# Kernel tuning notes

Hardware: AMD Instinct MI355X
Metric: run time of the kernel (lower is better)

The kernel has to match this reference:

```python
import jax, jax.numpy as jnp
import numpy as np

RADIUS = 0.1
MAX_GRID_DIM = 96
MAX_COLLISIONS = 128
INCLUDE_SELF = True


def setup_inputs() -> dict:
    key = jax.random.key(0)
    k1, k2, k3 = jax.random.split(key, 3)
    B, N, M, D, C = 2, 8192, 8192, 3, 64
    locs = jax.random.uniform(k1, (B, N, D), dtype=jnp.float32)
    data = jax.random.normal(k2, (B, N, C), dtype=jnp.float32)
    qlocs = jax.random.uniform(k3, (B, M, D), dtype=jnp.float32)
    return {"locs": locs, "data": data, "qlocs": qlocs}


def _hashgrid_order(locs):
    """Returns idxs [B,N] int32 sorting particles by flattened hash-grid cell id.
       idxs[b,i] = original index of the particle at new position i."""
    lower = jnp.min(locs, axis=1, keepdims=True)          # [B,1,D]
    upper = jnp.max(locs, axis=1, keepdims=True)          # [B,1,D]
    # grid dims per batch/dim, cell width = radius, capped at max_grid_dim
    gd = jnp.clip(jnp.floor((upper - lower) / RADIUS).astype(jnp.int32) + 1,
                  1, MAX_GRID_DIM)                        # [B,1,D]
    cell = jnp.floor((locs - lower) / RADIUS).astype(jnp.int32)
    cell = jnp.clip(cell, 0, gd - 1)                      # [B,N,D]
    # mixed-radix flatten: stride[d] = prod(gd[d+1:])
    strides = jnp.concatenate(
        [jnp.cumprod(gd[..., ::-1], axis=-1)[..., ::-1][..., 1:],
         jnp.ones_like(gd[..., :1])], axis=-1)            # [B,1,D]
    cid = jnp.sum(cell * strides, axis=-1)                # [B,N]
    return jnp.argsort(cid, axis=1, stable=True).astype(jnp.int32)


def _collisions(qlocs, nlocs):
    """For each query, indices into reordered locs within RADIUS, lowest-index
       first, padded with -1 up to MAX_COLLISIONS. Returns [B,M,K] int32."""
    B, N, _ = nlocs.shape
    d2 = jnp.sum((qlocs[:, :, None, :] - nlocs[:, None, :, :]) ** 2, axis=-1)  # [B,M,N]
    mask = d2 <= RADIUS * RADIUS
    if not INCLUDE_SELF:
        mask = mask & (d2 > 0)
    # key = particle index if neighbor else N (sentinel); first K after sort
    key = jnp.where(mask, jnp.arange(N, dtype=jnp.int32)[None, None, :], N)
    first_k = jnp.sort(key, axis=-1)[..., :MAX_COLLISIONS]                     # [B,M,K]
    return jnp.where(first_k < N, first_k, -1).astype(jnp.int32)


def reference(locs, data, qlocs):
    idxs = _hashgrid_order(locs)                              # [B,N]
    nlocs = jnp.take_along_axis(locs, idxs[..., None], axis=1)   # reordered locs
    ndata = jnp.take_along_axis(data, idxs[..., None], axis=1)   # reordered data
    neighbors = _collisions(qlocs, nlocs)                     # [B,M,K]
    return nlocs, ndata, idxs, neighbors
```

## Files before the change

kernel.cpp:

```cpp
#include <hip/hip_runtime.h>
#include <cfloat>
#include <math.h>

#define BB 2
#define NN 8192
#define MM 8192
#define CC 64
#define RAD 0.1f
#define R2 0.01f
#define MAXK 128
#define CELL_CAP 4096
#define CS_STRIDE 4100

#define WS_HDR 0
#define WS_SIDX 32
#define WS_CS (WS_SIDX + BB*NN)

#define NEIGH_BLOCKS ((BB*MM*16)/256)
#define DATA_BLOCKS ((BB*NN*16)/256)
#define NLOC_BLOCKS ((BB*NN)/256)

__device__ __forceinline__ int cell_of(float v, float lo, int g) {
    int c = (int)floorf(__fdiv_rn(v - lo, RAD));
    return min(max(c, 0), g - 1);
}

__global__ __launch_bounds__(1024) void build_kernel(const float* __restrict__ locs,
                                                     int* __restrict__ ws,
                                                     float* __restrict__ idxs_out) {
    const int b = blockIdx.x;
    const int t = threadIdx.x;
    const int lane = t & 63;
    const int wid = t >> 6;
    __shared__ int s_start[CELL_CAP + 1];
    __shared__ int s_aux[16];
    __shared__ int s_tmp[NN];
    __shared__ int s_cid[NN];
    __shared__ float s_red6[16 * 6];
    __shared__ float s_lo[3];
    __shared__ int   s_g[3];
    __shared__ int   s_str[2];

    const float* L = locs + (size_t)b * NN * 3;

    float mn0 = FLT_MAX, mn1 = FLT_MAX, mn2 = FLT_MAX;
    float mx0 = -FLT_MAX, mx1 = -FLT_MAX, mx2 = -FLT_MAX;
    for (int i = t; i < NN; i += 1024) {
        float x = L[i*3+0], y = L[i*3+1], z = L[i*3+2];
        mn0 = fminf(mn0, x); mx0 = fmaxf(mx0, x);
        mn1 = fminf(mn1, y); mx1 = fmaxf(mx1, y);
        mn2 = fminf(mn2, z); mx2 = fmaxf(mx2, z);
    }
    #pragma unroll
    for (int d = 1; d < 64; d <<= 1) {
        mn0 = fminf(mn0, __shfl_xor(mn0, d, 64));
        mn1 = fminf(mn1, __shfl_xor(mn1, d, 64));
        mn2 = fminf(mn2, __shfl_xor(mn2, d, 64));
        mx0 = fmaxf(mx0, __shfl_xor(mx0, d, 64));
        mx1 = fmaxf(mx1, __shfl_xor(mx1, d, 64));
        mx2 = fmaxf(mx2, __shfl_xor(mx2, d, 64));
    }
    if (lane == 0) {
        s_red6[wid*6+0] = mn0; s_red6[wid*6+1] = mn1; s_red6[wid*6+2] = mn2;
        s_red6[wid*6+3] = mx0; s_red6[wid*6+4] = mx1; s_red6[wid*6+5] = mx2;
    }
    for (int c = t; c < CELL_CAP + 1; c += 1024) s_start[c] = 0;
    __syncthreads();
    if (t == 0) {
        float lo0 = FLT_MAX, lo1 = FLT_MAX, lo2 = FLT_MAX;
        float up0 = -FLT_MAX, up1 = -FLT_MAX, up2 = -FLT_MAX;
        for (int w = 0; w < 16; ++w) {
            lo0 = fminf(lo0, s_red6[w*6+0]); lo1 = fminf(lo1, s_red6[w*6+1]);
            lo2 = fminf(lo2, s_red6[w*6+2]);
            up0 = fmaxf(up0, s_red6[w*6+3]); up1 = fmaxf(up1, s_red6[w*6+4]);
            up2 = fmaxf(up2, s_red6[w*6+5]);
        }
        int g0 = min(max((int)floorf(__fdiv_rn(up0 - lo0, RAD)) + 1, 1), 96);
        int g1 = min(max((int)floorf(__fdiv_rn(up1 - lo1, RAD)) + 1, 1), 96);
        int g2 = min(max((int)floorf(__fdiv_rn(up2 - lo2, RAD)) + 1, 1), 96);
        s_lo[0] = lo0; s_lo[1] = lo1; s_lo[2] = lo2;
        s_g[0] = g0; s_g[1] = g1; s_g[2] = g2;
        s_str[0] = g1 * g2; s_str[1] = g2;
        int* hdr = ws + WS_HDR + b * 16;
        hdr[0] = __float_as_int(lo0); hdr[1] = __float_as_int(lo1); hdr[2] = __float_as_int(lo2);
        hdr[3] = g0; hdr[4] = g1; hdr[5] = g2;
        hdr[6] = g1 * g2; hdr[7] = g2; hdr[8] = g0 * g1 * g2;
    }
    __syncthreads();
    const float lo0 = s_lo[0], lo1 = s_lo[1], lo2f = s_lo[2];
    const int g0 = s_g[0], g1 = s_g[1], g2 = s_g[2];
    const int st0 = s_str[0], st1 = s_str[1];
    const int ncells = g0 * g1 * g2;

    for (int i = t; i < NN; i += 1024) {
        int c0 = cell_of(L[i*3+0], lo0, g0);
        int c1 = cell_of(L[i*3+1], lo1, g1);
        int c2 = cell_of(L[i*3+2], lo2f, g2);
        int cid = c0*st0 + c1*st1 + c2;
        s_cid[i] = cid;
        atomicAdd(&s_start[cid], 1);
    }
    __syncthreads();

    int base4 = t * 4;
    int v0 = s_start[base4], v1 = s_start[base4+1], v2 = s_start[base4+2], v3 = s_start[base4+3];
    int sum = v0 + v1 + v2 + v3;
    int x = sum;
    #pragma unroll
    for (int d = 1; d < 64; d <<= 1) {
        int v = __shfl_up(x, d, 64);
        if (lane >= d) x += v;
    }
    if (lane == 63) s_aux[wid] = x;
    __syncthreads();
    if (wid == 0) {
        int w = (lane < 16) ? s_aux[lane] : 0;
        #pragma unroll
        for (int d = 1; d < 16; d <<= 1) {
            int v = __shfl_up(w, d, 64);
            if (lane >= d) w += v;
        }
        if (lane < 16) s_aux[lane] = w;
    }
    __syncthreads();
    int waveoff = (wid == 0) ? 0 : s_aux[wid - 1];
    int run = waveoff + x - sum;
    s_start[base4]   = run;
    s_start[base4+1] = run + v0;
    s_start[base4+2] = run + v0 + v1;
    s_start[base4+3] = run + v0 + v1 + v2;
    if (t == 1023) s_start[CELL_CAP] = run + sum;
    __syncthreads();

    for (int i = t; i < NN; i += 1024) {
        int pos = atomicAdd(&s_start[s_cid[i]], 1);
        s_tmp[pos] = i;
    }
    __syncthreads();

    int* cs = ws + WS_CS + b * CS_STRIDE;
    for (int c = t; c <= ncells; c += 1024) cs[c] = (c == 0) ? 0 : s_start[c - 1];

    int* sIdx = ws + WS_SIDX + b * NN;
    for (int p = t; p < NN; p += 1024) {
        int i = s_tmp[p];
        int cid = s_cid[i];
        int segs = (cid == 0) ? 0 : s_start[cid - 1];
        int sege = s_start[cid];
        int rank = 0;
        for (int q = segs; q < sege; ++q) rank += (s_tmp[q] < i) ? 1 : 0;
        int f = segs + rank;
        sIdx[f] = i;
        idxs_out[b * NN + f] = (float)i;
    }
}

__global__ __launch_bounds__(256) void fused_kernel(const float4* __restrict__ data4,
                                                    const float* __restrict__ locs,
                                                    const float* __restrict__ qlocs,
                                                    const int* __restrict__ ws,
                                                    float4* __restrict__ ndata4,
                                                    float* __restrict__ nlocs_out,
                                                    float* __restrict__ neigh_out) {
    int bid = blockIdx.x;
    if (bid >= NEIGH_BLOCKS) {
        int gb = bid - NEIGH_BLOCKS;
        if (gb < DATA_BLOCKS) {
            int tid = gb * 256 + threadIdx.x;
            int b = tid >> 17;
            int r = tid & ((NN * 16) - 1);
            int p = r >> 4;
            int c4 = r & 15;
            int idx = ws[WS_SIDX + b * NN + p];
            ndata4[tid] = data4[(((size_t)b * NN + idx) << 4) + c4];
        } else {
            int u = (gb - DATA_BLOCKS) * 256 + threadIdx.x;
            int b = u >> 13;
            int p = u & (NN - 1);
            int idx = ws[WS_SIDX + b * NN + p];
            const float* Lp = locs + ((size_t)b * NN + idx) * 3;
            float x = Lp[0], y = Lp[1], z = Lp[2];
            size_t o3 = ((size_t)b * NN + p) * 3;
            nlocs_out[o3+0] = x; nlocs_out[o3+1] = y; nlocs_out[o3+2] = z;
        }
        return;
    }
    const int tid  = bid * 256 + threadIdx.x;
    const int q    = tid >> 4;
    const int lane = threadIdx.x & 63;
    const int sub  = lane >> 4;
    const int lg   = lane & 15;
    const int b    = q >> 13;

    const int* hdr = ws + WS_HDR + b * 16;
    float lo0 = __int_as_float(hdr[0]);
    float lo1 = __int_as_float(hdr[1]);
    float lo2f = __int_as_float(hdr[2]);
    int g0 = hdr[3], g1 = hdr[4], g2 = hdr[5];
    int st0 = hdr[6], st1 = hdr[7];
    const int* cs = ws + WS_CS + b * CS_STRIDE;
    const int* sidx = ws + WS_SIDX + b * NN;
    const float* L = locs + (size_t)b * NN * 3;

    float qx = qlocs[(size_t)q * 3 + 0];
    float qy = qlocs[(size_t)q * 3 + 1];
    float qz = qlocs[(size_t)q * 3 + 2];

    int c0 = (int)floorf(__fdiv_rn(qx - lo0, RAD));
    int c1 = (int)floorf(__fdiv_rn(qy - lo1, RAD));
    int c2 = (int)floorf(__fdiv_rn(qz - lo2f, RAD));
    int a2lo = max(c2 - 1, 0), a2hi = min(c2 + 1, g2 - 1);
    bool zok = (a2lo <= a2hi);

    int rs[9], re[9];
    #pragma unroll
    for (int da0 = 0; da0 < 3; ++da0) {
        #pragma unroll
        for (int da1 = 0; da1 < 3; ++da1) {
            int k = da0 * 3 + da1;
            int a0 = c0 + da0 - 1;
            int a1 = c1 + da1 - 1;
            bool ok = zok && (a0 >= 0) && (a0 < g0) && (a1 >= 0) && (a1 < g1);
            int basec = a0 * st0 + a1 * st1;
            rs[k] = ok ? cs[basec + a2lo] : 0;
            re[k] = ok ? cs[basec + a2hi + 1] : 0;
        }
    }

    int cnt = 0;
    float* o = neigh_out + (size_t)q * MAXK;
    #pragma unroll
    for (int k = 0; k < 9; ++k) {
        int ps = rs[k], pe = re[k];
        for (int base = ps; base < pe; base += 16) {
            int p = base + lg;
            bool hit = false;
            if (p < pe) {
                int idx = sidx[p];
                const float* Lp = L + idx * 3;
                float dx = qx - Lp[0];
                float dy = qy - Lp[1];
                float dz = qz - Lp[2];
                float d2 = __fadd_rn(__fadd_rn(__fmul_rn(dx, dx), __fmul_rn(dy, dy)),
                                     __fmul_rn(dz, dz));
                hit = (d2 <= R2);
            }
            unsigned long long m = __ballot(hit);
            unsigned mb = (unsigned)((m >> (sub * 16)) & 0xFFFFull);
            if (hit) {
                int slot = cnt + __popc(mb & ((1u << lg) - 1u));
                if (slot < MAXK) o[slot] = (float)p;
            }
            cnt += __popc(mb);
        }
    }
    for (int s = cnt + lg; s < MAXK; s += 16) o[s] = -1.0f;
}

extern "C" void kernel_launch(void* const* d_in, const int* in_sizes, int n_in,
                              void* d_out, int out_size, void* d_ws, size_t ws_size,
                              hipStream_t stream) {
    (void)in_sizes; (void)n_in; (void)out_size; (void)ws_size;
    const float* locs  = (const float*)d_in[0];
    const float* data  = (const float*)d_in[1];
    const float* qlocs = (const float*)d_in[2];
    float* out = (float*)d_out;
    float* nlocs_out = out;
    float* ndata_out = out + BB * NN * 3;
    float* idxs_out  = out + BB * NN * 3 + BB * NN * CC;
    float* neigh_out = idxs_out + BB * NN;
    int* wsi = (int*)d_ws;

    build_kernel<<<BB, 1024, 0, stream>>>(locs, wsi, idxs_out);
    fused_kernel<<<NEIGH_BLOCKS + DATA_BLOCKS + NLOC_BLOCKS, 256, 0, stream>>>(
        (const float4*)data, locs, qlocs, wsi,
        (float4*)ndata_out, nlocs_out, neigh_out);
}
```

Measured before the change: 96.20 us.

## Emit reordered float4 positions in build kernel and drop the indirect neighbor gather

```diff
diff --git a/kernel.cpp b/kernel.cpp
--- a/kernel.cpp
+++ b/kernel.cpp
@@ -15,10 +15,10 @@
 #define WS_HDR 0
 #define WS_SIDX 32
 #define WS_CS (WS_SIDX + BB*NN)
+#define WS_NL4 (WS_CS + BB*CS_STRIDE)
 
 #define NEIGH_BLOCKS ((BB*MM*16)/256)
 #define DATA_BLOCKS ((BB*NN*16)/256)
-#define NLOC_BLOCKS ((BB*NN)/256)
 
 __device__ __forceinline__ int cell_of(float v, float lo, int g) {
     int c = (int)floorf(__fdiv_rn(v - lo, RAD));
@@ -27,15 +27,17 @@
 
 __global__ __launch_bounds__(1024) void build_kernel(const float* __restrict__ locs,
                                                      int* __restrict__ ws,
-                                                     float* __restrict__ idxs_out) {
+                                                     float* __restrict__ idxs_out,
+                                                     float* __restrict__ nlocs_out,
+                                                     float4* __restrict__ nlocs4) {
     const int b = blockIdx.x;
     const int t = threadIdx.x;
     const int lane = t & 63;
     const int wid = t >> 6;
+    __shared__ float s_x[NN], s_y[NN], s_z[NN];
     __shared__ int s_start[CELL_CAP + 1];
+    __shared__ int s_tmp[NN];
     __shared__ int s_aux[16];
-    __shared__ int s_tmp[NN];
-    __shared__ int s_cid[NN];
     __shared__ float s_red6[16 * 6];
     __shared__ float s_lo[3];
     __shared__ int   s_g[3];
@@ -47,6 +49,7 @@
     float mx0 = -FLT_MAX, mx1 = -FLT_MAX, mx2 = -FLT_MAX;
     for (int i = t; i < NN; i += 1024) {
         float x = L[i*3+0], y = L[i*3+1], z = L[i*3+2];
+        s_x[i] = x; s_y[i] = y; s_z[i] = z;
         mn0 = fminf(mn0, x); mx0 = fmaxf(mx0, x);
         mn1 = fminf(mn1, y); mx1 = fmaxf(mx1, y);
         mn2 = fminf(mn2, z); mx2 = fmaxf(mx2, z);
@@ -93,12 +96,10 @@
     const int ncells = g0 * g1 * g2;
 
     for (int i = t; i < NN; i += 1024) {
-        int c0 = cell_of(L[i*3+0], lo0, g0);
-        int c1 = cell_of(L[i*3+1], lo1, g1);
-        int c2 = cell_of(L[i*3+2], lo2f, g2);
-        int cid = c0*st0 + c1*st1 + c2;
-        s_cid[i] = cid;
-        atomicAdd(&s_start[cid], 1);
+        int c0 = cell_of(s_x[i], lo0, g0);
+        int c1 = cell_of(s_y[i], lo1, g1);
+        int c2 = cell_of(s_z[i], lo2f, g2);
+        atomicAdd(&s_start[c0*st0 + c1*st1 + c2], 1);
     }
     __syncthreads();
 
@@ -129,11 +130,13 @@
     s_start[base4+1] = run + v0;
     s_start[base4+2] = run + v0 + v1;
     s_start[base4+3] = run + v0 + v1 + v2;
-    if (t == 1023) s_start[CELL_CAP] = run + sum;
     __syncthreads();
 
     for (int i = t; i < NN; i += 1024) {
-        int pos = atomicAdd(&s_start[s_cid[i]], 1);
+        int c0 = cell_of(s_x[i], lo0, g0);
+        int c1 = cell_of(s_y[i], lo1, g1);
+        int c2 = cell_of(s_z[i], lo2f, g2);
+        int pos = atomicAdd(&s_start[c0*st0 + c1*st1 + c2], 1);
         s_tmp[pos] = i;
     }
     __syncthreads();
@@ -144,7 +147,11 @@
     int* sIdx = ws + WS_SIDX + b * NN;
     for (int p = t; p < NN; p += 1024) {
         int i = s_tmp[p];
-        int cid = s_cid[i];
+        float xi = s_x[i], yi = s_y[i], zi = s_z[i];
+        int c0 = cell_of(xi, lo0, g0);
+        int c1 = cell_of(yi, lo1, g1);
+        int c2 = cell_of(zi, lo2f, g2);
+        int cid = c0*st0 + c1*st1 + c2;
         int segs = (cid == 0) ? 0 : s_start[cid - 1];
         int sege = s_start[cid];
         int rank = 0;
@@ -152,37 +159,27 @@
         int f = segs + rank;
         sIdx[f] = i;
         idxs_out[b * NN + f] = (float)i;
+        size_t o3 = ((size_t)b * NN + f) * 3;
+        nlocs_out[o3+0] = xi; nlocs_out[o3+1] = yi; nlocs_out[o3+2] = zi;
+        nlocs4[(size_t)b * NN + f] = make_float4(xi, yi, zi, 0.0f);
     }
 }
 
 __global__ __launch_bounds__(256) void fused_kernel(const float4* __restrict__ data4,
-                                                    const float* __restrict__ locs,
                                                     const float* __restrict__ qlocs,
                                                     const int* __restrict__ ws,
                                                     float4* __restrict__ ndata4,
-                                                    float* __restrict__ nlocs_out,
+                                                    const float4* __restrict__ nlocs4,
                                                     float* __restrict__ neigh_out) {
     int bid = blockIdx.x;
     if (bid >= NEIGH_BLOCKS) {
-        int gb = bid - NEIGH_BLOCKS;
-        if (gb < DATA_BLOCKS) {
-            int tid = gb * 256 + threadIdx.x;
-            int b = tid >> 17;
-            int r = tid & ((NN * 16) - 1);
-            int p = r >> 4;
-            int c4 = r & 15;
-            int idx = ws[WS_SIDX + b * NN + p];
-            ndata4[tid] = data4[(((size_t)b * NN + idx) << 4) + c4];
-        } else {
-            int u = (gb - DATA_BLOCKS) * 256 + threadIdx.x;
-            int b = u >> 13;
-            int p = u & (NN - 1);
-            int idx = ws[WS_SIDX + b * NN + p];
-            const float* Lp = locs + ((size_t)b * NN + idx) * 3;
-            float x = Lp[0], y = Lp[1], z = Lp[2];
-            size_t o3 = ((size_t)b * NN + p) * 3;
-            nlocs_out[o3+0] = x; nlocs_out[o3+1] = y; nlocs_out[o3+2] = z;
-        }
+        int tid = (bid - NEIGH_BLOCKS) * 256 + threadIdx.x;
+        int b = tid >> 17;
+        int r = tid & ((NN * 16) - 1);
+        int p = r >> 4;
+        int c4 = r & 15;
+        int idx = ws[WS_SIDX + b * NN + p];
+        ndata4[tid] = data4[(((size_t)b * NN + idx) << 4) + c4];
         return;
     }
     const int tid  = bid * 256 + threadIdx.x;
@@ -199,8 +196,7 @@
     int g0 = hdr[3], g1 = hdr[4], g2 = hdr[5];
     int st0 = hdr[6], st1 = hdr[7];
     const int* cs = ws + WS_CS + b * CS_STRIDE;
-    const int* sidx = ws + WS_SIDX + b * NN;
-    const float* L = locs + (size_t)b * NN * 3;
+    const float4* P = nlocs4 + (size_t)b * NN;
 
     float qx = qlocs[(size_t)q * 3 + 0];
     float qy = qlocs[(size_t)q * 3 + 1];
@@ -236,11 +232,10 @@
             int p = base + lg;
             bool hit = false;
             if (p < pe) {
-                int idx = sidx[p];
-                const float* Lp = L + idx * 3;
-                float dx = qx - Lp[0];
-                float dy = qy - Lp[1];
-                float dz = qz - Lp[2];
+                float4 v = P[p];
+                float dx = qx - v.x;
+                float dy = qy - v.y;
+                float dz = qz - v.z;
                 float d2 = __fadd_rn(__fadd_rn(__fmul_rn(dx, dx), __fmul_rn(dy, dy)),
                                      __fmul_rn(dz, dz));
                 hit = (d2 <= R2);
@@ -270,9 +265,10 @@
     float* idxs_out  = out + BB * NN * 3 + BB * NN * CC;
     float* neigh_out = idxs_out + BB * NN;
     int* wsi = (int*)d_ws;
-
-    build_kernel<<<BB, 1024, 0, stream>>>(locs, wsi, idxs_out);
-    fused_kernel<<<NEIGH_BLOCKS + DATA_BLOCKS + NLOC_BLOCKS, 256, 0, stream>>>(
-        (const float4*)data, locs, qlocs, wsi,
-        (float4*)ndata_out, nlocs_out, neigh_out);
-}
+    float4* nlocs4 = (float4*)(wsi + WS_NL4);
+
+    build_kernel<<<BB, 1024, 0, stream>>>(locs, wsi, idxs_out, nlocs_out, nlocs4);
+    fused_kernel<<<NEIGH_BLOCKS + DATA_BLOCKS, 256, 0, stream>>>(
+        (const float4*)data, qlocs, wsi,
+        (float4*)ndata_out, nlocs4, neigh_out);
+}
```

Measured after the change: 94.89 us. About the same (-1.4%).
